# Performance work log

Hardware: AMD Instinct MI355X
Metric: run time of the kernel (lower is better)

The kernel has to match this reference:

```python
import jax, jax.numpy as jnp
import numpy as np

BN_EPS = 1e-5


def setup_inputs() -> dict:
    key = jax.random.key(0)
    ks = jax.random.split(key, 4)
    N, V, C = 64, 512, 512
    K, OUT = 2, 512
    x = jax.random.normal(ks[0], (N, V, C), dtype=jnp.float32)
    A = jax.random.uniform(ks[1], (N, K, V, V), dtype=jnp.float32) / V
    conv_w = jax.random.normal(ks[2], (2 * OUT, C), dtype=jnp.float32) / np.sqrt(C)
    conv_b = jax.random.normal(ks[3], (2 * OUT,), dtype=jnp.float32) * 0.01
    gamma = jnp.ones((2 * OUT,), dtype=jnp.float32)
    beta = jnp.zeros((2 * OUT,), dtype=jnp.float32)
    eps_p = jnp.zeros((1,), dtype=jnp.float32)
    return {"x": x, "A": A, "conv_w": conv_w, "conv_b": conv_b,
            "gamma": gamma, "beta": beta, "eps_p": eps_p}


def reference(x, A, conv_w, conv_b, gamma, beta, eps_p):
    # x: (N, V, C); A: (N, K, V, V)
    N, V, C = x.shape
    K = A.shape[1]
    # 1x1 Conv1d over nodes: (N, 2*out, V)
    h = jnp.einsum('nvc,oc->nov', x, conv_w) + conv_b[None, :, None]
    # BatchNorm1d, training-mode batch stats (biased variance, per channel)
    mean = jnp.mean(h, axis=(0, 2), keepdims=True)
    var = jnp.var(h, axis=(0, 2), keepdims=True)
    h = (h - mean) * jax.lax.rsqrt(var + BN_EPS) * gamma[None, :, None] + beta[None, :, None]
    c2 = h.shape[1]
    h = h.reshape(N, K, c2 // K, V)  # (N, K, out, V)
    # graph propagation: x A then (x A) A^T, contracted over node dims
    t = jnp.einsum('nkcm,nkme->nkce', h, A)
    At = jnp.transpose(A, (0, 1, 3, 2))
    y = jnp.einsum('nkce,nkem->ncm', t, At)  # (N, out, V)
    out = (1.0 + eps_p[0]) * x + jnp.transpose(y, (0, 2, 1))
    return out, At
```

## Files before the change

kernel.cpp:

```cpp
#include <hip/hip_runtime.h>
#include <stdint.h>

typedef __bf16 bf16x8 __attribute__((ext_vector_type(8)));
typedef float f32x4 __attribute__((ext_vector_type(4)));
typedef unsigned short us8_t __attribute__((ext_vector_type(8)));

__device__ __forceinline__ unsigned short f2bf(float f) {
  __bf16 b = (__bf16)f;
  return __builtin_bit_cast(unsigned short, b);
}
__device__ __forceinline__ float bf2f(unsigned short u) {
  union { uint32_t u; float f; } v; v.u = ((uint32_t)u) << 16;
  return v.f;
}

__device__ __forceinline__ void gload16(const void* g, void* l) {
  __builtin_amdgcn_global_load_lds(
      (const __attribute__((address_space(1))) void*)g,
      (__attribute__((address_space(3))) void*)l, 16, 0, 0);
}

__device__ __forceinline__ void stage_tile(const unsigned short* g, size_t ldg,
                                           unsigned short* lds, int wid, int lane) {
#pragma unroll
  for (int i = 0; i < 2; ++i) {
    int seg = wid * 2 + i;
    const unsigned short* gp = g + (size_t)(seg * 16 + (lane >> 2)) * ldg + (lane & 3) * 8;
    gload16(gp, lds + seg * 512);
  }
}

__device__ __forceinline__ void mfma_step(const unsigned short* As, const unsigned short* Bs,
                                          int ldb, f32x4 (*acc)[4],
                                          int wr, int wc, int lr, int lk) {
  bf16x8 a[4], b[4];
#pragma unroll
  for (int mi = 0; mi < 4; ++mi)
    a[mi] = *(const bf16x8*)(As + (wr + mi * 16 + lr) * 32 + lk * 8);
#pragma unroll
  for (int ni = 0; ni < 4; ++ni)
    b[ni] = *(const bf16x8*)(Bs + (wc + ni * 16 + lr) * ldb + lk * 8);
#pragma unroll
  for (int mi = 0; mi < 4; ++mi)
#pragma unroll
    for (int ni = 0; ni < 4; ++ni)
      acc[mi][ni] = __builtin_amdgcn_mfma_f32_16x16x32_bf16(a[mi], b[ni], acc[mi][ni], 0, 0, 0);
}

__global__ __launch_bounds__(256) void k_convert(
    const float* __restrict__ X, const float* __restrict__ W,
    unsigned short* __restrict__ Xb, unsigned short* __restrict__ Wb) {
  const size_t idx = (size_t)blockIdx.x * 256 + threadIdx.x;
  const size_t stride = (size_t)gridDim.x * 256;
  for (size_t i = idx; i < (size_t)16777216 / 8; i += stride) {
    float4 f0 = ((const float4*)X)[2 * i], f1 = ((const float4*)X)[2 * i + 1];
    us8_t w = { f2bf(f0.x), f2bf(f0.y), f2bf(f0.z), f2bf(f0.w),
                f2bf(f1.x), f2bf(f1.y), f2bf(f1.z), f2bf(f1.w) };
    ((us8_t*)Xb)[i] = w;
  }
  for (size_t i = idx; i < (size_t)524288 / 8; i += stride) {
    float4 f0 = ((const float4*)W)[2 * i], f1 = ((const float4*)W)[2 * i + 1];
    us8_t w = { f2bf(f0.x), f2bf(f0.y), f2bf(f0.z), f2bf(f0.w),
                f2bf(f1.x), f2bf(f1.y), f2bf(f1.z), f2bf(f1.w) };
    ((us8_t*)Wb)[i] = w;
  }
}

__global__ __launch_bounds__(256) void k_convertA(
    const float* __restrict__ A, unsigned short* __restrict__ Ab) {
  const size_t idx = (size_t)blockIdx.x * 256 + threadIdx.x;
  const size_t stride = (size_t)gridDim.x * 256;
  for (size_t i = idx; i < (size_t)33554432 / 8; i += stride) {
    float4 f0 = ((const float4*)A)[2 * i], f1 = ((const float4*)A)[2 * i + 1];
    us8_t w = { f2bf(f0.x), f2bf(f0.y), f2bf(f0.z), f2bf(f0.w),
                f2bf(f1.x), f2bf(f1.y), f2bf(f1.z), f2bf(f1.w) };
    ((us8_t*)Ab)[i] = w;
  }
}

__global__ __launch_bounds__(256) void k_gemm1(
    const unsigned short* __restrict__ Wb, const unsigned short* __restrict__ Xb,
    const float* __restrict__ convb, unsigned short* __restrict__ H) {
  __shared__ unsigned short A0[4096], B0[4096], A1[4096], B1[4096];
  const int tid = threadIdx.x;
  const int L = blockIdx.x;
  const int xcd = L & 7, slot = L >> 3;
  const int n = xcd * 8 + (slot >> 5);
  const int tile = slot & 31;
  const int tm = tile >> 2, tn = tile & 3;
  const unsigned short* gA = Wb + (size_t)tm * 128 * 512;
  const unsigned short* gB = Xb + ((size_t)n * 512 + tn * 128) * 512;
  const int lane = tid & 63, wid = tid >> 6;
  const int wr = (wid >> 1) * 64, wc = (wid & 1) * 64;
  const int lr = lane & 15, lk = lane >> 4;
  f32x4 acc[4][4] = {};
  stage_tile(gA, 512, A0, wid, lane);
  stage_tile(gB, 512, B0, wid, lane);
  for (int k0 = 0; k0 < 512; k0 += 64) {
    __syncthreads();
    stage_tile(gA + k0 + 32, 512, A1, wid, lane);
    stage_tile(gB + k0 + 32, 512, B1, wid, lane);
    mfma_step(A0, B0, 32, acc, wr, wc, lr, lk);
    __syncthreads();
    if (k0 + 64 < 512) {
      stage_tile(gA + k0 + 64, 512, A0, wid, lane);
      stage_tile(gB + k0 + 64, 512, B0, wid, lane);
    }
    mfma_step(A1, B1, 32, acc, wr, wc, lr, lk);
  }
  unsigned short* Hn = H + (size_t)n * 1024 * 512;
#pragma unroll
  for (int mi = 0; mi < 4; ++mi)
#pragma unroll
    for (int i = 0; i < 4; ++i) {
      int o = tm * 128 + wr + mi * 16 + lk * 4 + i;
      float bias = convb[o];
#pragma unroll
      for (int ni = 0; ni < 4; ++ni) {
        int v = tn * 128 + wc + ni * 16 + lr;
        Hn[(size_t)o * 512 + v] = f2bf(acc[mi][ni][i] + bias);
      }
    }
}

__global__ __launch_bounds__(256) void k_bn(
    const unsigned short* __restrict__ H, const float* __restrict__ gamma,
    const float* __restrict__ beta, float* __restrict__ sc_sh) {
  const int o = blockIdx.x;
  const int tid = threadIdx.x;
  const int g = tid >> 6, l = tid & 63;
  float s1 = 0.f, s2 = 0.f;
  for (int step = 0; step < 16; ++step) {
    int n = g + step * 4;
    const us8_t* row = (const us8_t*)(H + ((size_t)n * 1024 + o) * 512);
    us8_t v = row[l];
#pragma unroll
    for (int j = 0; j < 8; ++j) { float f = bf2f(v[j]); s1 += f; s2 += f * f; }
  }
  __shared__ float r1[256], r2[256];
  r1[tid] = s1; r2[tid] = s2;
  __syncthreads();
  for (int off = 128; off > 0; off >>= 1) {
    if (tid < off) { r1[tid] += r1[tid + off]; r2[tid] += r2[tid + off]; }
    __syncthreads();
  }
  if (tid == 0) {
    float mean = r1[0] * (1.0f / 32768.0f);
    float var = r2[0] * (1.0f / 32768.0f) - mean * mean;
    float s = gamma[o] * rsqrtf(var + 1e-5f);
    sc_sh[o] = s;
    sc_sh[1024 + o] = beta[o] - mean * s;
  }
}

__global__ __launch_bounds__(256) void k_affine(
    unsigned short* __restrict__ H, const float* __restrict__ sc_sh) {
  const size_t idx = (size_t)blockIdx.x * 256 + threadIdx.x;
  const size_t stride = (size_t)gridDim.x * 256;
  const size_t total8 = (size_t)64 * 1024 * 512 / 8;
  for (size_t i = idx; i < total8; i += stride) {
    size_t base = i * 8;
    int o = (int)((base >> 9) & 1023);
    float sc = sc_sh[o], sh = sc_sh[1024 + o];
    us8_t v = ((const us8_t*)H)[i];
    us8_t w;
#pragma unroll
    for (int j = 0; j < 8; ++j) w[j] = f2bf(fmaf(bf2f(v[j]), sc, sh));
    ((us8_t*)H)[i] = w;
  }
}

__global__ __launch_bounds__(256) void k_aat(
    const unsigned short* __restrict__ Ab, unsigned short* __restrict__ B2) {
  __shared__ unsigned short A0[4096], B0[4096], A1[4096], B1[4096];
  const int tid = threadIdx.x;
  const int L = blockIdx.x;
  const int xcd = L & 7, slot = L >> 3;
  const int nk = xcd * 16 + (slot >> 4);
  const int tile = slot & 15;
  const int tm = tile >> 2, tn = tile & 3;
  const unsigned short* Ank = Ab + (size_t)nk * 262144;
  const unsigned short* gA = Ank + (size_t)tm * 128 * 512;
  const unsigned short* gB = Ank + (size_t)tn * 128 * 512;
  const int lane = tid & 63, wid = tid >> 6;
  const int wr = (wid >> 1) * 64, wc = (wid & 1) * 64;
  const int lr = lane & 15, lk = lane >> 4;
  f32x4 acc[4][4] = {};
  stage_tile(gA, 512, A0, wid, lane);
  stage_tile(gB, 512, B0, wid, lane);
  for (int k0 = 0; k0 < 512; k0 += 64) {
    __syncthreads();
    stage_tile(gA + k0 + 32, 512, A1, wid, lane);
    stage_tile(gB + k0 + 32, 512, B1, wid, lane);
    mfma_step(A0, B0, 32, acc, wr, wc, lr, lk);
    __syncthreads();
    if (k0 + 64 < 512) {
      stage_tile(gA + k0 + 64, 512, A0, wid, lane);
      stage_tile(gB + k0 + 64, 512, B0, wid, lane);
    }
    mfma_step(A1, B1, 32, acc, wr, wc, lr, lk);
  }
  unsigned short* Bn = B2 + (size_t)nk * 262144;
#pragma unroll
  for (int mi = 0; mi < 4; ++mi)
#pragma unroll
    for (int i = 0; i < 4; ++i) {
      int m = tm * 128 + wr + mi * 16 + lk * 4 + i;
#pragma unroll
      for (int ni = 0; ni < 4; ++ni) {
        int mp = tn * 128 + wc + ni * 16 + lr;
        Bn[(size_t)m * 512 + mp] = f2bf(acc[mi][ni][i]);
      }
    }
}

__device__ __forceinline__ void ldB(const unsigned short* gB, int k, int tid,
                                    us8_t* va, us8_t* vb) {
  int r0 = tid >> 2, c8 = (tid & 3) * 8;
  *va = *(const us8_t*)(gB + (size_t)r0 * 512 + k + c8);
  *vb = *(const us8_t*)(gB + (size_t)(r0 + 64) * 512 + k + c8);
}

template <bool AFFINE>
__device__ __forceinline__ void wrB(unsigned short* Bs, us8_t va, us8_t vb,
                                    float scA, float shA, float scB, float shB,
                                    int tid) {
  int r0 = tid >> 2, c8 = (tid & 3) * 8;
  us8_t w;
  if (AFFINE) {
#pragma unroll
    for (int j = 0; j < 8; ++j) w[j] = f2bf(fmaf(bf2f(va[j]), scA, shA));
  } else w = va;
  *(us8_t*)&Bs[r0 * 40 + c8] = w;
  if (AFFINE) {
#pragma unroll
    for (int j = 0; j < 8; ++j) w[j] = f2bf(fmaf(bf2f(vb[j]), scB, shB));
  } else w = vb;
  *(us8_t*)&Bs[(r0 + 64) * 40 + c8] = w;
}

template <bool AFFINE>
__global__ __launch_bounds__(256) void k_gemm3(
    const unsigned short* __restrict__ B2, const unsigned short* __restrict__ H,
    const float* __restrict__ sc_sh, const float* __restrict__ X,
    const float* __restrict__ epsp, float* __restrict__ out) {
  __shared__ unsigned short A0[4096], A1[4096];
  __shared__ unsigned short Bs0[128 * 40], Bs1[128 * 40];
  const int tid = threadIdx.x;
  const int L = blockIdx.x;
  const int xcd = L & 7, slot = L >> 3;
  const int n = xcd * 8 + (slot >> 4);
  const int tile = slot & 15;
  const int tm = tile >> 2, tn = tile & 3;
  const int lane = tid & 63, wid = tid >> 6;
  const int wr = (wid >> 1) * 64, wc = (wid & 1) * 64;
  const int lr = lane & 15, lk = lane >> 4;
  f32x4 acc[4][4] = {};
  for (int kk = 0; kk < 2; ++kk) {
    const unsigned short* gA = B2 + ((size_t)(n * 2 + kk) * 512 + tm * 128) * 512;
    const unsigned short* gB = H + ((size_t)n * 1024 + kk * 512 + tn * 128) * 512;
    float scA = 0.f, shA = 0.f, scB = 0.f, shB = 0.f;
    if (AFFINE) {
      int r0 = tid >> 2;
      int ch = kk * 512 + tn * 128;
      scA = sc_sh[ch + r0];       shA = sc_sh[1024 + ch + r0];
      scB = sc_sh[ch + r0 + 64];  shB = sc_sh[1024 + ch + r0 + 64];
    }
    us8_t va, vb;
    ldB(gB, 0, tid, &va, &vb);
    stage_tile(gA, 512, A0, wid, lane);
    wrB<AFFINE>(Bs0, va, vb, scA, shA, scB, shB, tid);
    for (int k0 = 0; k0 < 512; k0 += 64) {
      __syncthreads();
      stage_tile(gA + k0 + 32, 512, A1, wid, lane);
      ldB(gB, k0 + 32, tid, &va, &vb);
      mfma_step(A0, Bs0, 40, acc, wr, wc, lr, lk);
      wrB<AFFINE>(Bs1, va, vb, scA, shA, scB, shB, tid);
      __syncthreads();
      const bool more = (k0 + 64 < 512);
      if (more) {
        stage_tile(gA + k0 + 64, 512, A0, wid, lane);
        ldB(gB, k0 + 64, tid, &va, &vb);
      }
      mfma_step(A1, Bs1, 40, acc, wr, wc, lr, lk);
      if (more) wrB<AFFINE>(Bs0, va, vb, scA, shA, scB, shB, tid);
    }
  }
  const float e1 = 1.0f + epsp[0];
#pragma unroll
  for (int mi = 0; mi < 4; ++mi)
#pragma unroll
    for (int i = 0; i < 4; ++i) {
      int v = tm * 128 + wr + mi * 16 + lk * 4 + i;
#pragma unroll
      for (int ni = 0; ni < 4; ++ni) {
        int c = tn * 128 + wc + ni * 16 + lr;
        size_t idx = ((size_t)n * 512 + v) * 512 + c;
        out[idx] = fmaf(e1, X[idx], acc[mi][ni][i]);
      }
    }
}

__global__ __launch_bounds__(256) void k_at(
    const float* __restrict__ A, float* __restrict__ At) {
  __shared__ float tile[64][65];
  const int nk = blockIdx.z;
  const int e0 = blockIdx.x * 64, m0 = blockIdx.y * 64;
  const float* src = A + (size_t)nk * 262144;
  float* dst = At + (size_t)nk * 262144;
  const int t = threadIdx.x;
#pragma unroll
  for (int j = 0; j < 4; ++j) {
    int ch = t + j * 256;
    int r = ch >> 4, c4 = (ch & 15) * 4;
    float4 f = *(const float4*)(src + (size_t)(m0 + r) * 512 + e0 + c4);
    tile[r][c4] = f.x; tile[r][c4 + 1] = f.y; tile[r][c4 + 2] = f.z; tile[r][c4 + 3] = f.w;
  }
  __syncthreads();
#pragma unroll
  for (int j = 0; j < 4; ++j) {
    int ch = t + j * 256;
    int e = ch >> 4, m4 = (ch & 15) * 4;
    float4 g = { tile[m4][e], tile[m4 + 1][e], tile[m4 + 2][e], tile[m4 + 3][e] };
    *(float4*)(dst + (size_t)(e0 + e) * 512 + m0 + m4) = g;
  }
}

extern "C" void kernel_launch(void* const* d_in, const int* in_sizes, int n_in,
                              void* d_out, int out_size, void* d_ws, size_t ws_size,
                              hipStream_t stream) {
  const float* x      = (const float*)d_in[0];
  const float* A      = (const float*)d_in[1];
  const float* conv_w = (const float*)d_in[2];
  const float* conv_b = (const float*)d_in[3];
  const float* gamma  = (const float*)d_in[4];
  const float* beta   = (const float*)d_in[5];
  const float* eps_p  = (const float*)d_in[6];

  float* out = (float*)d_out;
  float* At  = out + (size_t)16777216;

  unsigned short* B2 = (unsigned short*)At;
  unsigned short* H  = (unsigned short*)(At + (size_t)16777216);
  unsigned short* Xb = (unsigned short*)out;
  unsigned short* Wb = Xb + (size_t)16777216;
  unsigned short* Ab = (unsigned short*)out;

  float* wsf = (float*)d_ws;

  if (ws_size >= 8192) {
    float* sc_sh = wsf;
    k_convert    <<<2048, 256, 0, stream>>>(x, conv_w, Xb, Wb);
    k_gemm1      <<<2048, 256, 0, stream>>>(Wb, Xb, conv_b, H);
    k_bn         <<<1024, 256, 0, stream>>>(H, gamma, beta, sc_sh);
    k_convertA   <<<2048, 256, 0, stream>>>(A, Ab);
    k_aat        <<<2048, 256, 0, stream>>>(Ab, B2);
    k_gemm3<true><<<1024, 256, 0, stream>>>(B2, H, sc_sh, x, eps_p, out);
  } else {
    float* sc_sh = out;
    k_convert     <<<2048, 256, 0, stream>>>(x, conv_w, Xb, Wb);
    k_gemm1       <<<2048, 256, 0, stream>>>(Wb, Xb, conv_b, H);
    k_bn          <<<1024, 256, 0, stream>>>(H, gamma, beta, sc_sh);
    k_affine      <<<2048, 256, 0, stream>>>(H, sc_sh);
    k_convertA    <<<2048, 256, 0, stream>>>(A, Ab);
    k_aat         <<<2048, 256, 0, stream>>>(Ab, B2);
    k_gemm3<false><<<1024, 256, 0, stream>>>(B2, H, nullptr, x, eps_p, out);
  }
  k_at<<<dim3(8, 8, 128), 256, 0, stream>>>(A, At);
}
```

Before: 324.3 us.

## Single-buffer GEMM loops, fuse BN stats with A conversion, cache BN params in LDS

All three GEMM kernels drop their double-buffered LDS prefetch in favour of a simple load, sync, compute, sync loop with 32-wide K steps. The BN statistics kernel and the A-to-bf16 conversion are merged into one launch with 3072 blocks, saving a kernel launch and letting both run concurrently. In gemm3, the per-channel scale and shift are staged once in shared memory, and the B tile is loaded and transformed in place. Halving LDS use may allow more resident blocks, but the loads are no longer overlapped with MFMA work, which risks exposing memory latency.

```diff
diff --git a/kernel.cpp b/kernel.cpp
--- a/kernel.cpp
+++ b/kernel.cpp
@@ -4,6 +4,8 @@
 typedef __bf16 bf16x8 __attribute__((ext_vector_type(8)));
 typedef float f32x4 __attribute__((ext_vector_type(4)));
 typedef unsigned short us8_t __attribute__((ext_vector_type(8)));
+
+#define LDSK 40
 
 __device__ __forceinline__ unsigned short f2bf(float f) {
   __bf16 b = (__bf16)f;
@@ -66,22 +68,11 @@
   }
 }
 
-__global__ __launch_bounds__(256) void k_convertA(
-    const float* __restrict__ A, unsigned short* __restrict__ Ab) {
-  const size_t idx = (size_t)blockIdx.x * 256 + threadIdx.x;
-  const size_t stride = (size_t)gridDim.x * 256;
-  for (size_t i = idx; i < (size_t)33554432 / 8; i += stride) {
-    float4 f0 = ((const float4*)A)[2 * i], f1 = ((const float4*)A)[2 * i + 1];
-    us8_t w = { f2bf(f0.x), f2bf(f0.y), f2bf(f0.z), f2bf(f0.w),
-                f2bf(f1.x), f2bf(f1.y), f2bf(f1.z), f2bf(f1.w) };
-    ((us8_t*)Ab)[i] = w;
-  }
-}
-
 __global__ __launch_bounds__(256) void k_gemm1(
     const unsigned short* __restrict__ Wb, const unsigned short* __restrict__ Xb,
     const float* __restrict__ convb, unsigned short* __restrict__ H) {
-  __shared__ unsigned short A0[4096], B0[4096], A1[4096], B1[4096];
+  __shared__ unsigned short As[4096];
+  __shared__ unsigned short Bs[4096];
   const int tid = threadIdx.x;
   const int L = blockIdx.x;
   const int xcd = L & 7, slot = L >> 3;
@@ -94,19 +85,12 @@
   const int wr = (wid >> 1) * 64, wc = (wid & 1) * 64;
   const int lr = lane & 15, lk = lane >> 4;
   f32x4 acc[4][4] = {};
-  stage_tile(gA, 512, A0, wid, lane);
-  stage_tile(gB, 512, B0, wid, lane);
-  for (int k0 = 0; k0 < 512; k0 += 64) {
-    __syncthreads();
-    stage_tile(gA + k0 + 32, 512, A1, wid, lane);
-    stage_tile(gB + k0 + 32, 512, B1, wid, lane);
-    mfma_step(A0, B0, 32, acc, wr, wc, lr, lk);
-    __syncthreads();
-    if (k0 + 64 < 512) {
-      stage_tile(gA + k0 + 64, 512, A0, wid, lane);
-      stage_tile(gB + k0 + 64, 512, B0, wid, lane);
-    }
-    mfma_step(A1, B1, 32, acc, wr, wc, lr, lk);
+  for (int k0 = 0; k0 < 512; k0 += 32) {
+    stage_tile(gA + k0, 512, As, wid, lane);
+    stage_tile(gB + k0, 512, Bs, wid, lane);
+    __syncthreads();
+    mfma_step(As, Bs, 32, acc, wr, wc, lr, lk);
+    __syncthreads();
   }
   unsigned short* Hn = H + (size_t)n * 1024 * 512;
 #pragma unroll
@@ -121,6 +105,48 @@
         Hn[(size_t)o * 512 + v] = f2bf(acc[mi][ni][i] + bias);
       }
     }
+}
+
+__global__ __launch_bounds__(256) void k_bn_convA(
+    const unsigned short* __restrict__ H, const float* __restrict__ gamma,
+    const float* __restrict__ beta, float* __restrict__ sc_sh,
+    const float* __restrict__ A, unsigned short* __restrict__ Ab) {
+  const int tid = threadIdx.x;
+  if (blockIdx.x < 1024) {
+    const int o = blockIdx.x;
+    const int g = tid >> 6, l = tid & 63;
+    float s1 = 0.f, s2 = 0.f;
+    for (int step = 0; step < 16; ++step) {
+      int n = g + step * 4;
+      const us8_t* row = (const us8_t*)(H + ((size_t)n * 1024 + o) * 512);
+      us8_t v = row[l];
+#pragma unroll
+      for (int j = 0; j < 8; ++j) { float f = bf2f(v[j]); s1 += f; s2 += f * f; }
+    }
+    __shared__ float r1[256], r2[256];
+    r1[tid] = s1; r2[tid] = s2;
+    __syncthreads();
+    for (int off = 128; off > 0; off >>= 1) {
+      if (tid < off) { r1[tid] += r1[tid + off]; r2[tid] += r2[tid + off]; }
+      __syncthreads();
+    }
+    if (tid == 0) {
+      float mean = r1[0] * (1.0f / 32768.0f);
+      float var = r2[0] * (1.0f / 32768.0f) - mean * mean;
+      float s = gamma[o] * rsqrtf(var + 1e-5f);
+      sc_sh[o] = s;
+      sc_sh[1024 + o] = beta[o] - mean * s;
+    }
+  } else {
+    const size_t idx = (size_t)(blockIdx.x - 1024) * 256 + tid;
+    const size_t stride = (size_t)2048 * 256;
+    for (size_t i = idx; i < (size_t)33554432 / 8; i += stride) {
+      float4 f0 = ((const float4*)A)[2 * i], f1 = ((const float4*)A)[2 * i + 1];
+      us8_t w = { f2bf(f0.x), f2bf(f0.y), f2bf(f0.z), f2bf(f0.w),
+                  f2bf(f1.x), f2bf(f1.y), f2bf(f1.z), f2bf(f1.w) };
+      ((us8_t*)Ab)[i] = w;
+    }
+  }
 }
 
 __global__ __launch_bounds__(256) void k_bn(
@@ -150,6 +176,18 @@
     float s = gamma[o] * rsqrtf(var + 1e-5f);
     sc_sh[o] = s;
     sc_sh[1024 + o] = beta[o] - mean * s;
+  }
+}
+
+__global__ __launch_bounds__(256) void k_convertA(
+    const float* __restrict__ A, unsigned short* __restrict__ Ab) {
+  const size_t idx = (size_t)blockIdx.x * 256 + threadIdx.x;
+  const size_t stride = (size_t)gridDim.x * 256;
+  for (size_t i = idx; i < (size_t)33554432 / 8; i += stride) {
+    float4 f0 = ((const float4*)A)[2 * i], f1 = ((const float4*)A)[2 * i + 1];
+    us8_t w = { f2bf(f0.x), f2bf(f0.y), f2bf(f0.z), f2bf(f0.w),
+                f2bf(f1.x), f2bf(f1.y), f2bf(f1.z), f2bf(f1.w) };
+    ((us8_t*)Ab)[i] = w;
   }
 }
 
@@ -172,7 +210,8 @@
 
 __global__ __launch_bounds__(256) void k_aat(
     const unsigned short* __restrict__ Ab, unsigned short* __restrict__ B2) {
-  __shared__ unsigned short A0[4096], B0[4096], A1[4096], B1[4096];
+  __shared__ unsigned short As[4096];
+  __shared__ unsigned short Bs[4096];
   const int tid = threadIdx.x;
   const int L = blockIdx.x;
   const int xcd = L & 7, slot = L >> 3;
@@ -186,19 +225,12 @@
   const int wr = (wid >> 1) * 64, wc = (wid & 1) * 64;
   const int lr = lane & 15, lk = lane >> 4;
   f32x4 acc[4][4] = {};
-  stage_tile(gA, 512, A0, wid, lane);
-  stage_tile(gB, 512, B0, wid, lane);
-  for (int k0 = 0; k0 < 512; k0 += 64) {
-    __syncthreads();
-    stage_tile(gA + k0 + 32, 512, A1, wid, lane);
-    stage_tile(gB + k0 + 32, 512, B1, wid, lane);
-    mfma_step(A0, B0, 32, acc, wr, wc, lr, lk);
-    __syncthreads();
-    if (k0 + 64 < 512) {
-      stage_tile(gA + k0 + 64, 512, A0, wid, lane);
-      stage_tile(gB + k0 + 64, 512, B0, wid, lane);
-    }
-    mfma_step(A1, B1, 32, acc, wr, wc, lr, lk);
+  for (int k0 = 0; k0 < 512; k0 += 32) {
+    stage_tile(gA + k0, 512, As, wid, lane);
+    stage_tile(gB + k0, 512, Bs, wid, lane);
+    __syncthreads();
+    mfma_step(As, Bs, 32, acc, wr, wc, lr, lk);
+    __syncthreads();
   }
   unsigned short* Bn = B2 + (size_t)nk * 262144;
 #pragma unroll
@@ -212,31 +244,6 @@
         Bn[(size_t)m * 512 + mp] = f2bf(acc[mi][ni][i]);
       }
     }
-}
-
-__device__ __forceinline__ void ldB(const unsigned short* gB, int k, int tid,
-                                    us8_t* va, us8_t* vb) {
-  int r0 = tid >> 2, c8 = (tid & 3) * 8;
-  *va = *(const us8_t*)(gB + (size_t)r0 * 512 + k + c8);
-  *vb = *(const us8_t*)(gB + (size_t)(r0 + 64) * 512 + k + c8);
-}
-
-template <bool AFFINE>
-__device__ __forceinline__ void wrB(unsigned short* Bs, us8_t va, us8_t vb,
-                                    float scA, float shA, float scB, float shB,
-                                    int tid) {
-  int r0 = tid >> 2, c8 = (tid & 3) * 8;
-  us8_t w;
-  if (AFFINE) {
-#pragma unroll
-    for (int j = 0; j < 8; ++j) w[j] = f2bf(fmaf(bf2f(va[j]), scA, shA));
-  } else w = va;
-  *(us8_t*)&Bs[r0 * 40 + c8] = w;
-  if (AFFINE) {
-#pragma unroll
-    for (int j = 0; j < 8; ++j) w[j] = f2bf(fmaf(bf2f(vb[j]), scB, shB));
-  } else w = vb;
-  *(us8_t*)&Bs[(r0 + 64) * 40 + c8] = w;
 }
 
 template <bool AFFINE>
@@ -244,8 +251,9 @@
     const unsigned short* __restrict__ B2, const unsigned short* __restrict__ H,
     const float* __restrict__ sc_sh, const float* __restrict__ X,
     const float* __restrict__ epsp, float* __restrict__ out) {
-  __shared__ unsigned short A0[4096], A1[4096];
-  __shared__ unsigned short Bs0[128 * 40], Bs1[128 * 40];
+  __shared__ unsigned short As[4096];
+  __shared__ unsigned short Bs[128 * LDSK];
+  __shared__ float s_sc[2][128], s_sh[2][128];
   const int tid = threadIdx.x;
   const int L = blockIdx.x;
   const int xcd = L & 7, slot = L >> 3;
@@ -255,35 +263,38 @@
   const int lane = tid & 63, wid = tid >> 6;
   const int wr = (wid >> 1) * 64, wc = (wid & 1) * 64;
   const int lr = lane & 15, lk = lane >> 4;
+  if (AFFINE) {
+    if (tid < 256) {
+      int kkq = tid >> 7, r = tid & 127;
+      s_sc[kkq][r] = sc_sh[kkq * 512 + tn * 128 + r];
+      s_sh[kkq][r] = sc_sh[1024 + kkq * 512 + tn * 128 + r];
+    }
+    __syncthreads();
+  }
   f32x4 acc[4][4] = {};
   for (int kk = 0; kk < 2; ++kk) {
     const unsigned short* gA = B2 + ((size_t)(n * 2 + kk) * 512 + tm * 128) * 512;
     const unsigned short* gB = H + ((size_t)n * 1024 + kk * 512 + tn * 128) * 512;
-    float scA = 0.f, shA = 0.f, scB = 0.f, shB = 0.f;
-    if (AFFINE) {
-      int r0 = tid >> 2;
-      int ch = kk * 512 + tn * 128;
-      scA = sc_sh[ch + r0];       shA = sc_sh[1024 + ch + r0];
-      scB = sc_sh[ch + r0 + 64];  shB = sc_sh[1024 + ch + r0 + 64];
-    }
-    us8_t va, vb;
-    ldB(gB, 0, tid, &va, &vb);
-    stage_tile(gA, 512, A0, wid, lane);
-    wrB<AFFINE>(Bs0, va, vb, scA, shA, scB, shB, tid);
-    for (int k0 = 0; k0 < 512; k0 += 64) {
+    for (int k0 = 0; k0 < 512; k0 += 32) {
+      stage_tile(gA + k0, 512, As, wid, lane);
+#pragma unroll
+      for (int i = 0; i < 2; ++i) {
+        int s = tid + i * 256;
+        int r = s >> 2, c8 = (s & 3) * 8;
+        us8_t v = *(const us8_t*)(gB + (size_t)r * 512 + k0 + c8);
+        if (AFFINE) {
+          float sc = s_sc[kk][r], sh = s_sh[kk][r];
+          us8_t w;
+#pragma unroll
+          for (int j = 0; j < 8; ++j) w[j] = f2bf(fmaf(bf2f(v[j]), sc, sh));
+          *(us8_t*)&Bs[r * LDSK + c8] = w;
+        } else {
+          *(us8_t*)&Bs[r * LDSK + c8] = v;
+        }
+      }
       __syncthreads();
-      stage_tile(gA + k0 + 32, 512, A1, wid, lane);
-      ldB(gB, k0 + 32, tid, &va, &vb);
-      mfma_step(A0, Bs0, 40, acc, wr, wc, lr, lk);
-      wrB<AFFINE>(Bs1, va, vb, scA, shA, scB, shB, tid);
+      mfma_step(As, Bs, LDSK, acc, wr, wc, lr, lk);
       __syncthreads();
-      const bool more = (k0 + 64 < 512);
-      if (more) {
-        stage_tile(gA + k0 + 64, 512, A0, wid, lane);
-        ldB(gB, k0 + 64, tid, &va, &vb);
-      }
-      mfma_step(A1, Bs1, 40, acc, wr, wc, lr, lk);
-      if (more) wrB<AFFINE>(Bs0, va, vb, scA, shA, scB, shB, tid);
     }
   }
   const float e1 = 1.0f + epsp[0];
@@ -352,8 +363,7 @@
     float* sc_sh = wsf;
     k_convert    <<<2048, 256, 0, stream>>>(x, conv_w, Xb, Wb);
     k_gemm1      <<<2048, 256, 0, stream>>>(Wb, Xb, conv_b, H);
-    k_bn         <<<1024, 256, 0, stream>>>(H, gamma, beta, sc_sh);
-    k_convertA   <<<2048, 256, 0, stream>>>(A, Ab);
+    k_bn_convA   <<<3072, 256, 0, stream>>>(H, gamma, beta, sc_sh, A, Ab);
     k_aat        <<<2048, 256, 0, stream>>>(Ab, B2);
     k_gemm3<true><<<1024, 256, 0, stream>>>(B2, H, sc_sh, x, eps_p, out);
   } else {
```

Result: faster. 296.5 us (-8.6%).
